# Kernel tuning notes

Hardware: AMD Instinct MI355X
Metric: run time of the kernel (lower is better)

## Reference

```python
import jax, jax.numpy as jnp
import numpy as np

TAU = 0.07
EPS = 1e-6  # torch CosineSimilarity eps


def setup_inputs() -> dict:
    key = jax.random.key(0)
    k1, k2, k3 = jax.random.split(key, 3)
    n, d, n_classes = 8192, 256, 1024
    imitation_embeds = jax.random.normal(k1, (n, d), dtype=jnp.float32)
    recording_embeds = jax.random.normal(k2, (n, d), dtype=jnp.float32)
    labels = jax.random.randint(k3, (n,), 0, n_classes, dtype=jnp.int64)
    return {
        "imitation_embeds": imitation_embeds,
        "recording_embeds": recording_embeds,
        "labels": labels,
    }


def reference(imitation_embeds, recording_embeds, labels):
    n = imitation_embeds.shape[0]
    # cosine similarity with per-vector norm clamp (torch semantics)
    im_n = imitation_embeds / jnp.maximum(
        jnp.linalg.norm(imitation_embeds, axis=1, keepdims=True), EPS)
    rec_n = recording_embeds / jnp.maximum(
        jnp.linalg.norm(recording_embeds, axis=1, keepdims=True), EPS)
    i2r = jnp.einsum("nd,md->nm", im_n, rec_n) / TAU  # [n, n]

    same = labels[:, None] == labels[None, :]          # [n, n] bool
    eye = jnp.eye(n, dtype=bool)
    # original: mask = ~(same ^ diag_embed(diag(same))); diag(same) is all True
    # -> keep the diagonal (positive) and all different-label negatives
    mask = ~(same ^ eye)

    # per-row masked log-softmax evaluated at the diagonal entry:
    # log_softmax(row[mask])[pos_of_diag] = i2r[i,i] - logsumexp(row over mask)
    lse = jax.nn.logsumexp(jnp.where(mask, i2r, -jnp.inf), axis=1)  # [n]
    loss = -jnp.mean(jnp.diagonal(i2r) - lse)
    return loss
```

## Files before the change

### kernel.cpp

```cpp
#include <hip/hip_runtime.h>

#define N 8192
#define D 256
#define INV_TAU 14.285714285714286f
#define LOG2E 1.4426950408889634f
#define EPSN 1e-6f

#define RT 128
#define CT 32
#define CSPLIT 16
#define CPB (N / CSPLIT)
#define NTILES (CPB / CT)
#define MAXC 96

typedef unsigned int u32x4 __attribute__((ext_vector_type(4)));
typedef __bf16 bf16x8 __attribute__((ext_vector_type(8)));
typedef float f32x4 __attribute__((ext_vector_type(4)));

__device__ inline unsigned short f2bf(float x) {
    unsigned int u = __builtin_bit_cast(unsigned int, x);
    u += 0x7fffu + ((u >> 16) & 1u);
    return (unsigned short)(u >> 16);
}

__device__ inline float bf2f(unsigned short u) {
    return __builtin_bit_cast(float, (unsigned int)u << 16);
}

__global__ void ntx_prep(const float* __restrict__ im, const float* __restrict__ rec,
                         unsigned short* __restrict__ A, unsigned short* __restrict__ Bm,
                         float* __restrict__ diag, float* __restrict__ rowsum,
                         int* __restrict__ cnt, float* __restrict__ out) {
    const int wave = threadIdx.x >> 6;
    const int lane = threadIdx.x & 63;
    const int row  = blockIdx.x * 4 + wave;

    const float4 a = ((const float4*)(im  + (size_t)row * D))[lane];
    const float4 b = ((const float4*)(rec + (size_t)row * D))[lane];

    float ssa = a.x*a.x + a.y*a.y + a.z*a.z + a.w*a.w;
    float ssb = b.x*b.x + b.y*b.y + b.z*b.z + b.w*b.w;
    float dt  = a.x*b.x + a.y*b.y + a.z*b.z + a.w*b.w;
    #pragma unroll
    for (int o = 32; o; o >>= 1) {
        ssa += __shfl_xor(ssa, o);
        ssb += __shfl_xor(ssb, o);
        dt  += __shfl_xor(dt , o);
    }
    const float ra = 1.0f / fmaxf(sqrtf(ssa), EPSN);
    const float rb = 1.0f / fmaxf(sqrtf(ssb), EPSN);
    const float sa = ra * (INV_TAU * LOG2E);

    ushort4 pa, pb;
    pa.x = f2bf(a.x*sa); pa.y = f2bf(a.y*sa); pa.z = f2bf(a.z*sa); pa.w = f2bf(a.w*sa);
    pb.x = f2bf(b.x*rb); pb.y = f2bf(b.y*rb); pb.z = f2bf(b.z*rb); pb.w = f2bf(b.w*rb);
    *(ushort4*)(A  + (size_t)row * D + lane * 4) = pa;
    *(ushort4*)(Bm + (size_t)row * D + lane * 4) = pb;

    if (lane == 0) {
        diag[row]   = dt * ra * rb * INV_TAU;
        rowsum[row] = 0.0f;
    }
    if (blockIdx.x < 4) cnt[blockIdx.x * 256 + threadIdx.x] = 0;
    if (blockIdx.x == 0 && threadIdx.x == 0) out[0] = 0.0f;
}

__global__ void ntx_bucket(const int* __restrict__ labels, int* __restrict__ cnt,
                           int* __restrict__ bucket) {
    const int i = blockIdx.x * 256 + threadIdx.x;
    const int c = labels[i];
    const int pos = atomicAdd(&cnt[c], 1);
    if (pos < MAXC) bucket[c * MAXC + pos] = i;
}

__global__ void ntx_pairs(const unsigned short* __restrict__ A,
                          const unsigned short* __restrict__ Bm,
                          const int* __restrict__ labels,
                          const int* __restrict__ cnt, const int* __restrict__ bucket,
                          float* __restrict__ rowsum) {
    const int wave = threadIdx.x >> 6;
    const int lane = threadIdx.x & 63;
    const int i = blockIdx.x * 4 + wave;
    const int c = labels[i];
    const int m = min(cnt[c], MAXC);
    if (m < 2) return;

    const ushort4 av = *(const ushort4*)(A + (size_t)i * D + lane * 4);
    const float a0 = bf2f(av.x), a1 = bf2f(av.y), a2 = bf2f(av.z), a3 = bf2f(av.w);

    int jr_n = bucket[c * MAXC];
    ushort4 bv_n = *(const ushort4*)(Bm + (size_t)jr_n * D + lane * 4);

    float corr = 0.f;
    for (int j = 0; j < m; ++j) {
        const int jr = jr_n;
        const ushort4 bv = bv_n;
        if (j + 1 < m) {
            jr_n = bucket[c * MAXC + j + 1];
            bv_n = *(const ushort4*)(Bm + (size_t)jr_n * D + lane * 4);
        }
        if (jr == i) continue;
        float d = a0*bf2f(bv.x) + a1*bf2f(bv.y) + a2*bf2f(bv.z) + a3*bf2f(bv.w);
        #pragma unroll
        for (int o = 32; o; o >>= 1) d += __shfl_xor(d, o);
        corr += __builtin_amdgcn_exp2f(d);
    }
    if (lane == 0) atomicAdd(&rowsum[i], -corr);
}

__device__ __forceinline__ void stage_tile(const unsigned short* __restrict__ Bm,
                                           int colbase, int wave, int lane,
                                           unsigned char* lb) {
    const int g = lane >> 4, n16 = lane & 15;
    #pragma unroll
    for (int p = 0; p < 4; ++p) {
        const int csk = p * 4 + wave;
        const int cs = csk >> 3, k = csk & 7;
        const unsigned short* gs =
            Bm + (size_t)(colbase + cs * 16 + n16) * D + k * 32 + g * 8;
        __builtin_amdgcn_global_load_lds(
            (const __attribute__((address_space(1))) unsigned int*)gs,
            (__attribute__((address_space(3))) unsigned int*)(lb + csk * 1024),
            16, 0, 0);
    }
}

__global__ __launch_bounds__(256, 4)
void ntx_lse(const unsigned short* __restrict__ A, const unsigned short* __restrict__ Bm,
             float* __restrict__ rowsum) {
    __shared__ __align__(128) unsigned char Bs[2][CT * 512];

    const int wave = threadIdx.x >> 6;
    const int lane = threadIdx.x & 63;
    const int g    = lane >> 4;
    const int n16  = lane & 15;

    const int rowblk = blockIdx.x & (N / RT - 1);
    const int colblk = blockIdx.x >> 6;
    const int row0 = rowblk * RT + wave * 32;
    const int col0 = colblk * CPB;

    bf16x8 afrag[2][8];
    #pragma unroll
    for (int rs = 0; rs < 2; ++rs) {
        const int r = row0 + rs * 16 + n16;
        #pragma unroll
        for (int k = 0; k < 8; ++k)
            afrag[rs][k] = __builtin_bit_cast(
                bf16x8, *(const u32x4*)(A + (size_t)r * D + k * 32 + g * 8));
    }

    float acc[2][4] = {{0.f,0.f,0.f,0.f},{0.f,0.f,0.f,0.f}};

    stage_tile(Bm, col0, wave, lane, &Bs[0][0]);
    asm volatile("s_waitcnt vmcnt(0)" ::: "memory");
    __builtin_amdgcn_s_barrier();
    __builtin_amdgcn_sched_barrier(0);

    for (int t = 0; t < NTILES; ++t) {
        const int buf = t & 1;
        if (t + 1 < NTILES)
            stage_tile(Bm, col0 + (t + 1) * CT, wave, lane, &Bs[buf ^ 1][0]);

        #pragma unroll
        for (int cs = 0; cs < 2; ++cs) {
            bf16x8 bfrag[8];
            #pragma unroll
            for (int k = 0; k < 8; ++k)
                bfrag[k] = __builtin_bit_cast(
                    bf16x8, *(const u32x4*)(&Bs[buf][(cs * 8 + k) * 1024 + lane * 16]));

            #pragma unroll
            for (int rs = 0; rs < 2; ++rs) {
                f32x4 c = {0.f, 0.f, 0.f, 0.f};
                #pragma unroll
                for (int k = 0; k < 8; ++k)
                    c = __builtin_amdgcn_mfma_f32_16x16x32_bf16(
                            afrag[rs][k], bfrag[k], c, 0, 0, 0);
                #pragma unroll
                for (int q = 0; q < 4; ++q)
                    acc[rs][q] += __builtin_amdgcn_exp2f(c[q]);
            }
        }

        asm volatile("s_waitcnt vmcnt(0)" ::: "memory");
        __builtin_amdgcn_s_barrier();
        __builtin_amdgcn_sched_barrier(0);
    }

    #pragma unroll
    for (int rs = 0; rs < 2; ++rs)
        #pragma unroll
        for (int q = 0; q < 4; ++q) {
            float v = acc[rs][q];
            v += __shfl_xor(v, 1);
            v += __shfl_xor(v, 2);
            v += __shfl_xor(v, 4);
            v += __shfl_xor(v, 8);
            if (n16 == 0)
                atomicAdd(&rowsum[row0 + rs * 16 + g * 4 + q], v);
        }
}

__global__ void ntx_finish(const float* __restrict__ diag,
                           const float* __restrict__ rowsum,
                           float* __restrict__ out) {
    __shared__ float red[4];
    const int i = blockIdx.x * 256 + threadIdx.x;
    float s = logf(rowsum[i]) - diag[i];
    #pragma unroll
    for (int o = 32; o; o >>= 1) s += __shfl_xor(s, o);
    if ((threadIdx.x & 63) == 0) red[threadIdx.x >> 6] = s;
    __syncthreads();
    if (threadIdx.x == 0)
        atomicAdd(out, (red[0] + red[1] + red[2] + red[3]) * (1.0f / (float)N));
}

extern "C" void kernel_launch(void* const* d_in, const int* in_sizes, int n_in,
                              void* d_out, int out_size, void* d_ws, size_t ws_size,
                              hipStream_t stream) {
    const float* im     = (const float*)d_in[0];
    const float* rec    = (const float*)d_in[1];
    const int*   labels = (const int*)d_in[2];
    float* out = (float*)d_out;

    unsigned short* A  = (unsigned short*)d_ws;
    unsigned short* Bm = A + (size_t)N * D;
    float* diag   = (float*)(Bm + (size_t)N * D);
    float* rowsum = diag + N;
    int*   cnt    = (int*)(rowsum + N);
    int*   bucket = cnt + 1024;

    ntx_prep<<<N / 4, 256, 0, stream>>>(im, rec, A, Bm, diag, rowsum, cnt, out);
    ntx_bucket<<<N / 256, 256, 0, stream>>>(labels, cnt, bucket);
    ntx_pairs<<<N / 4, 256, 0, stream>>>(A, Bm, labels, cnt, bucket, rowsum);
    ntx_lse<<<(N / RT) * CSPLIT, 256, 0, stream>>>(A, Bm, rowsum);
    ntx_finish<<<N / 256, 256, 0, stream>>>(diag, rowsum, out);
}
```

Baseline: 127.8 us.

## Deepen LSE tile pipeline to 4 buffers and fuse pair correction into finish

The LSE kernel now keeps four LDS tile buffers with loads issued three tiles ahead, waits on partial vmcnt, and software-pipelines the work so the exp2 accumulation of one chunk overlaps the MFMAs of the next, with MFMAs bracketed by setprio. Column split is halved and launch bounds lowered to 2 waves per SIMD to fit the larger LDS. The same-label pair correction kernel is merged with the final reduction kernel, which removes one launch and one rowsum atomic pass. Lower occupancy and fewer blocks could reduce latency hiding, and the finish kernel now carries the gather work.

```diff
diff --git a/kernel.cpp b/kernel.cpp
--- a/kernel.cpp
+++ b/kernel.cpp
@@ -8,9 +8,10 @@
 
 #define RT 128
 #define CT 32
-#define CSPLIT 16
+#define CSPLIT 8
 #define CPB (N / CSPLIT)
 #define NTILES (CPB / CT)
+#define TILEB (CT * 512)
 #define MAXC 96
 
 typedef unsigned int u32x4 __attribute__((ext_vector_type(4)));
@@ -73,51 +74,16 @@
     if (pos < MAXC) bucket[c * MAXC + pos] = i;
 }
 
-__global__ void ntx_pairs(const unsigned short* __restrict__ A,
-                          const unsigned short* __restrict__ Bm,
-                          const int* __restrict__ labels,
-                          const int* __restrict__ cnt, const int* __restrict__ bucket,
-                          float* __restrict__ rowsum) {
-    const int wave = threadIdx.x >> 6;
-    const int lane = threadIdx.x & 63;
-    const int i = blockIdx.x * 4 + wave;
-    const int c = labels[i];
-    const int m = min(cnt[c], MAXC);
-    if (m < 2) return;
-
-    const ushort4 av = *(const ushort4*)(A + (size_t)i * D + lane * 4);
-    const float a0 = bf2f(av.x), a1 = bf2f(av.y), a2 = bf2f(av.z), a3 = bf2f(av.w);
-
-    int jr_n = bucket[c * MAXC];
-    ushort4 bv_n = *(const ushort4*)(Bm + (size_t)jr_n * D + lane * 4);
-
-    float corr = 0.f;
-    for (int j = 0; j < m; ++j) {
-        const int jr = jr_n;
-        const ushort4 bv = bv_n;
-        if (j + 1 < m) {
-            jr_n = bucket[c * MAXC + j + 1];
-            bv_n = *(const ushort4*)(Bm + (size_t)jr_n * D + lane * 4);
-        }
-        if (jr == i) continue;
-        float d = a0*bf2f(bv.x) + a1*bf2f(bv.y) + a2*bf2f(bv.z) + a3*bf2f(bv.w);
-        #pragma unroll
-        for (int o = 32; o; o >>= 1) d += __shfl_xor(d, o);
-        corr += __builtin_amdgcn_exp2f(d);
-    }
-    if (lane == 0) atomicAdd(&rowsum[i], -corr);
-}
-
-__device__ __forceinline__ void stage_tile(const unsigned short* __restrict__ Bm,
-                                           int colbase, int wave, int lane,
-                                           unsigned char* lb) {
+__device__ __forceinline__ void stage_tile4(const unsigned short* __restrict__ Bm,
+                                            int colt, int wave, int lane,
+                                            unsigned char* lb) {
     const int g = lane >> 4, n16 = lane & 15;
     #pragma unroll
     for (int p = 0; p < 4; ++p) {
-        const int csk = p * 4 + wave;
+        const int csk = wave * 4 + p;
         const int cs = csk >> 3, k = csk & 7;
         const unsigned short* gs =
-            Bm + (size_t)(colbase + cs * 16 + n16) * D + k * 32 + g * 8;
+            Bm + (size_t)(colt + cs * 16 + n16) * D + k * 32 + g * 8;
         __builtin_amdgcn_global_load_lds(
             (const __attribute__((address_space(1))) unsigned int*)gs,
             (__attribute__((address_space(3))) unsigned int*)(lb + csk * 1024),
@@ -125,10 +91,40 @@
     }
 }
 
-__global__ __launch_bounds__(256, 4)
+__device__ __forceinline__ void read_chunk(const unsigned char* buf, int cs, int lane,
+                                           bf16x8 (&bf)[8]) {
+    #pragma unroll
+    for (int k = 0; k < 8; ++k)
+        bf[k] = __builtin_bit_cast(
+            bf16x8, *(const u32x4*)(buf + (cs * 8 + k) * 1024 + lane * 16));
+}
+
+__device__ __forceinline__ void mfma_chunk(const bf16x8 (&afrag)[2][8],
+                                           const bf16x8 (&bf)[8], f32x4 (&cp)[2]) {
+    cp[0] = (f32x4){0.f, 0.f, 0.f, 0.f};
+    cp[1] = (f32x4){0.f, 0.f, 0.f, 0.f};
+    __builtin_amdgcn_s_setprio(1);
+    #pragma unroll
+    for (int k = 0; k < 8; ++k)
+        #pragma unroll
+        for (int rs = 0; rs < 2; ++rs)
+            cp[rs] = __builtin_amdgcn_mfma_f32_16x16x32_bf16(
+                         afrag[rs][k], bf[k], cp[rs], 0, 0, 0);
+    __builtin_amdgcn_s_setprio(0);
+}
+
+__device__ __forceinline__ void expacc(const f32x4 (&cp)[2], float (&acc)[2][4]) {
+    #pragma unroll
+    for (int rs = 0; rs < 2; ++rs)
+        #pragma unroll
+        for (int q = 0; q < 4; ++q)
+            acc[rs][q] += __builtin_amdgcn_exp2f(cp[rs][q]);
+}
+
+__global__ __launch_bounds__(256, 2)
 void ntx_lse(const unsigned short* __restrict__ A, const unsigned short* __restrict__ Bm,
              float* __restrict__ rowsum) {
-    __shared__ __align__(128) unsigned char Bs[2][CT * 512];
+    __shared__ __align__(128) unsigned char Bs[4][TILEB];
 
     const int wave = threadIdx.x >> 6;
     const int lane = threadIdx.x & 63;
@@ -152,41 +148,48 @@
 
     float acc[2][4] = {{0.f,0.f,0.f,0.f},{0.f,0.f,0.f,0.f}};
 
-    stage_tile(Bm, col0, wave, lane, &Bs[0][0]);
-    asm volatile("s_waitcnt vmcnt(0)" ::: "memory");
+    f32x4 cp[2];
+    cp[0] = (f32x4){-__builtin_huge_valf(), -__builtin_huge_valf(),
+                    -__builtin_huge_valf(), -__builtin_huge_valf()};
+    cp[1] = cp[0];
+
+    stage_tile4(Bm, col0 + 0 * CT, wave, lane, &Bs[0][0]);
+    stage_tile4(Bm, col0 + 1 * CT, wave, lane, &Bs[1][0]);
+    stage_tile4(Bm, col0 + 2 * CT, wave, lane, &Bs[2][0]);
+    asm volatile("s_waitcnt vmcnt(4)" ::: "memory");
     __builtin_amdgcn_s_barrier();
     __builtin_amdgcn_sched_barrier(0);
 
+    bf16x8 bfA[8], bfB[8];
+    read_chunk(&Bs[0][0], 0, lane, bfA);
+
     for (int t = 0; t < NTILES; ++t) {
-        const int buf = t & 1;
-        if (t + 1 < NTILES)
-            stage_tile(Bm, col0 + (t + 1) * CT, wave, lane, &Bs[buf ^ 1][0]);
-
-        #pragma unroll
-        for (int cs = 0; cs < 2; ++cs) {
-            bf16x8 bfrag[8];
+        #pragma unroll
+        for (int rs = 0; rs < 2; ++rs)
             #pragma unroll
             for (int k = 0; k < 8; ++k)
-                bfrag[k] = __builtin_bit_cast(
-                    bf16x8, *(const u32x4*)(&Bs[buf][(cs * 8 + k) * 1024 + lane * 16]));
-
-            #pragma unroll
-            for (int rs = 0; rs < 2; ++rs) {
-                f32x4 c = {0.f, 0.f, 0.f, 0.f};
-                #pragma unroll
-                for (int k = 0; k < 8; ++k)
-                    c = __builtin_amdgcn_mfma_f32_16x16x32_bf16(
-                            afrag[rs][k], bfrag[k], c, 0, 0, 0);
-                #pragma unroll
-                for (int q = 0; q < 4; ++q)
-                    acc[rs][q] += __builtin_amdgcn_exp2f(c[q]);
-            }
-        }
-
-        asm volatile("s_waitcnt vmcnt(0)" ::: "memory");
+                asm volatile("" : "+v"(afrag[rs][k]));
+
+        if (t + 3 < NTILES)
+            stage_tile4(Bm, col0 + (t + 3) * CT, wave, lane, &Bs[(t + 3) & 3][0]);
+
+        read_chunk(&Bs[t & 3][0], 1, lane, bfB);
+        expacc(cp, acc);
+        mfma_chunk(afrag, bfA, cp);
+
+        if (t + 1 < NTILES)
+            read_chunk(&Bs[(t + 1) & 3][0], 0, lane, bfA);
+        expacc(cp, acc);
+        mfma_chunk(afrag, bfB, cp);
+
+        if (t < NTILES - 4)
+            asm volatile("s_waitcnt vmcnt(4)" ::: "memory");
+        else
+            asm volatile("s_waitcnt vmcnt(0)" ::: "memory");
         __builtin_amdgcn_s_barrier();
         __builtin_amdgcn_sched_barrier(0);
     }
+    expacc(cp, acc);
 
     #pragma unroll
     for (int rs = 0; rs < 2; ++rs)
@@ -202,15 +205,43 @@
         }
 }
 
-__global__ void ntx_finish(const float* __restrict__ diag,
-                           const float* __restrict__ rowsum,
-                           float* __restrict__ out) {
+__global__ void ntx_pairsfin(const unsigned short* __restrict__ A,
+                             const unsigned short* __restrict__ Bm,
+                             const int* __restrict__ labels,
+                             const int* __restrict__ cnt, const int* __restrict__ bucket,
+                             const float* __restrict__ diag,
+                             const float* __restrict__ rowsum,
+                             float* __restrict__ out) {
     __shared__ float red[4];
-    const int i = blockIdx.x * 256 + threadIdx.x;
-    float s = logf(rowsum[i]) - diag[i];
-    #pragma unroll
-    for (int o = 32; o; o >>= 1) s += __shfl_xor(s, o);
-    if ((threadIdx.x & 63) == 0) red[threadIdx.x >> 6] = s;
+    const int wave = threadIdx.x >> 6;
+    const int lane = threadIdx.x & 63;
+    const int i = blockIdx.x * 4 + wave;
+    const int c = labels[i];
+    const int m = min(cnt[c], MAXC);
+
+    float corr = 0.f;
+    if (m >= 2) {
+        const ushort4 av = *(const ushort4*)(A + (size_t)i * D + lane * 4);
+        const float a0 = bf2f(av.x), a1 = bf2f(av.y), a2 = bf2f(av.z), a3 = bf2f(av.w);
+
+        int jr_n = bucket[c * MAXC];
+        ushort4 bv_n = *(const ushort4*)(Bm + (size_t)jr_n * D + lane * 4);
+
+        for (int j = 0; j < m; ++j) {
+            const int jr = jr_n;
+            const ushort4 bv = bv_n;
+            if (j + 1 < m) {
+                jr_n = bucket[c * MAXC + j + 1];
+                bv_n = *(const ushort4*)(Bm + (size_t)jr_n * D + lane * 4);
+            }
+            if (jr == i) continue;
+            float d = a0*bf2f(bv.x) + a1*bf2f(bv.y) + a2*bf2f(bv.z) + a3*bf2f(bv.w);
+            #pragma unroll
+            for (int o = 32; o; o >>= 1) d += __shfl_xor(d, o);
+            corr += __builtin_amdgcn_exp2f(d);
+        }
+    }
+    if (lane == 0) red[wave] = logf(rowsum[i] - corr) - diag[i];
     __syncthreads();
     if (threadIdx.x == 0)
         atomicAdd(out, (red[0] + red[1] + red[2] + red[3]) * (1.0f / (float)N));
@@ -233,7 +264,6 @@
 
     ntx_prep<<<N / 4, 256, 0, stream>>>(im, rec, A, Bm, diag, rowsum, cnt, out);
     ntx_bucket<<<N / 256, 256, 0, stream>>>(labels, cnt, bucket);
-    ntx_pairs<<<N / 4, 256, 0, stream>>>(A, Bm, labels, cnt, bucket, rowsum);
     ntx_lse<<<(N / RT) * CSPLIT, 256, 0, stream>>>(A, Bm, rowsum);
-    ntx_finish<<<N / 256, 256, 0, stream>>>(diag, rowsum, out);
-}
+    ntx_pairsfin<<<N / 4, 256, 0, stream>>>(A, Bm, labels, cnt, bucket, diag, rowsum, out);
+}
```

Result: slower. 143.5 us (+12.2%).
